# Kernel optimization log

Measured on AMD Instinct MI355X. Metric: run time of the kernel, lower is better.

Reference implementation:

```python
import jax, jax.numpy as jnp
import numpy as np
from jax import lax

K = 9
CENTER = K // 2
EXTEND = 1.0
EPS = 1e-5
GROUPS = 16  # out_ch // 4


def conv2d(x, w, b, stride, padding):
    y = lax.conv_general_dilated(x, w, window_strides=stride, padding=padding,
                                 dimension_numbers=('NCHW', 'OIHW', 'NCHW'))
    return y + b[None, :, None, None]


def setup_inputs() -> dict:
    key = jax.random.key(0)
    ks = jax.random.split(key, 9)
    B, C, Wd, Hd, OUT = 8, 64, 128, 128, 64
    f = jax.random.normal(ks[0], (B, C, Wd, Hd), jnp.float32)
    w_off = jax.random.normal(ks[1], (2 * K, C, 3, 3), jnp.float32) * 0.05
    b_off = jax.random.normal(ks[2], (2 * K,), jnp.float32) * 0.05
    bn_gamma = 1.0 + 0.1 * jax.random.normal(ks[3], (2 * K,), jnp.float32)
    bn_beta = 0.1 * jax.random.normal(ks[4], (2 * K,), jnp.float32)
    w_dsc = jax.random.normal(ks[5], (OUT, C, K, 1), jnp.float32) * 0.05
    b_dsc = jax.random.normal(ks[6], (OUT,), jnp.float32) * 0.05
    gn_gamma = 1.0 + 0.1 * jax.random.normal(ks[7], (OUT,), jnp.float32)
    gn_beta = 0.1 * jax.random.normal(ks[8], (OUT,), jnp.float32)
    return {'f': f, 'w_off': w_off, 'b_off': b_off, 'bn_gamma': bn_gamma,
            'bn_beta': bn_beta, 'w_dsc': w_dsc, 'b_dsc': b_dsc,
            'gn_gamma': gn_gamma, 'gn_beta': gn_beta}


def _forward(f, w_off, b_off, bn_gamma, bn_beta, w_dsc, b_dsc, gn_gamma, gn_beta):
    B, C, Wd, Hd = f.shape  # module names: width=shape[2], height=shape[3]
    dt = f.dtype

    # offset branch: conv3x3 -> BatchNorm (training mode, batch stats) -> tanh
    off = conv2d(f, w_off, b_off, (1, 1), 'SAME')
    mu = off.mean(axis=(0, 2, 3), keepdims=True)
    var = off.var(axis=(0, 2, 3), keepdims=True)
    off = (off - mu) / jnp.sqrt(var + EPS)
    off = off * bn_gamma[None, :, None, None] + bn_beta[None, :, None, None]
    off = jnp.tanh(off)

    y_off = off[:, :K]  # [B,K,Wd,Hd]; x_off (off[:, K:]) unused for morph=0

    # cumulative offset scan from the center point (morph=0).
    # NOTE: endpoints 0 and K-1 keep detached raw offsets (torch detach().clone()).
    raw0 = lax.stop_gradient(y_off)
    offn = [None] * K
    offn[CENTER] = jnp.zeros_like(y_off[:, 0])
    for i in range(1, CENTER):
        offn[CENTER + i] = offn[CENTER + i - 1] + y_off[:, CENTER + i]
        offn[CENTER - i] = offn[CENTER - i + 1] + y_off[:, CENTER - i]
    offn[0] = raw0[:, 0]
    offn[K - 1] = raw0[:, K - 1]
    offn = jnp.stack(offn, axis=1)  # [B,K,Wd,Hd]

    # coordinate grids: y indexes the width axis, x the height axis
    y_new = jnp.arange(Wd, dtype=dt)[None, None, :, None] + offn * EXTEND  # [B,K,Wd,Hd]
    x_new = ((jnp.arange(K, dtype=dt) - CENTER)[None, :, None, None]
             + jnp.arange(Hd, dtype=dt)[None, None, None, :])  # [1,K,1,Hd]
    x_new = jnp.broadcast_to(x_new, (B, K, Wd, Hd))

    # layout [B, K*Wd, Hd] via (B,K,Wd,Hd) -> (B,Wd,K,Hd)
    y_s = jnp.transpose(y_new, (0, 2, 1, 3)).reshape(B, K * Wd * Hd)
    x_s = jnp.transpose(x_new, (0, 2, 1, 3)).reshape(B, K * Wd * Hd)

    # bilinear interpolation (clamped corner indices, unclamped y/x in weights)
    y0 = jnp.floor(y_s).astype(jnp.int32)
    x0 = jnp.floor(x_s).astype(jnp.int32)
    y0c = jnp.clip(y0, 0, Wd - 1)
    y1c = jnp.clip(y0 + 1, 0, Wd - 1)
    x0c = jnp.clip(x0, 0, Hd - 1)
    x1c = jnp.clip(x0 + 1, 0, Hd - 1)

    feat = jnp.transpose(f, (0, 2, 3, 1)).reshape(B, Wd * Hd, C)

    def gather(yi, xi):
        idx = (yi * Hd + xi)[:, :, None]  # [B,N,1]
        return jnp.take_along_axis(feat, idx, axis=1)  # [B,N,C]

    va0 = gather(y0c, x0c)
    vc0 = gather(y0c, x1c)
    va1 = gather(y1c, x0c)
    vc1 = gather(y1c, x1c)

    y0f, y1f = y0c.astype(dt), y1c.astype(dt)
    x0f, x1f = x0c.astype(dt), x1c.astype(dt)
    wa = ((y1f - y_s) * (x1f - x_s))[:, :, None]
    wb = ((y1f - y_s) * (x_s - x0f))[:, :, None]
    wc = ((y_s - y0f) * (x1f - x_s))[:, :, None]
    wd = ((y_s - y0f) * (x_s - x0f))[:, :, None]

    out = va0 * wa + vc0 * wb + va1 * wc + vc1 * wd  # [B,N,C]
    deformed = jnp.transpose(out.reshape(B, K * Wd, Hd, C), (0, 3, 1, 2))  # [B,C,K*Wd,Hd]

    # strided conv over the K snake points -> [B,OUT,Wd,Hd]
    x = conv2d(deformed, w_dsc, b_dsc, (K, 1), 'VALID')

    # GroupNorm + ReLU
    OUT = x.shape[1]
    xg = x.reshape(B, GROUPS, -1)
    gmu = xg.mean(axis=-1, keepdims=True)
    gvar = xg.var(axis=-1, keepdims=True)
    xg = (xg - gmu) / jnp.sqrt(gvar + EPS)
    x = xg.reshape(x.shape) * gn_gamma[None, :, None, None] + gn_beta[None, :, None, None]
    return jax.nn.relu(x)


def reference(f, w_off, b_off, bn_gamma, bn_beta, w_dsc, b_dsc, gn_gamma, gn_beta):
    return _forward(f, w_off, b_off, bn_gamma, bn_beta, w_dsc, b_dsc, gn_gamma, gn_beta)
```

## Files before the change

kernel.cpp:

```cpp
#include <hip/hip_runtime.h>

#define B_   8
#define C_   64
#define W_   128
#define H_   128
#define K_   9
#define OUT_ 64
#define NPIX (B_*W_*H_)
#define EPS_ 1e-5f

typedef __attribute__((ext_vector_type(8))) short bf16x8;
typedef __attribute__((ext_vector_type(4))) float f32x4;

#define FEATBF_OFF  0
#define XPRE_OFF    4194304
#define OFFPRE_OFF  8388608
#define OFFH_OFF    9568256
#define WT_OFF      14286848
#define WP_OFF      14305280
#define BNSTATS_OFF 14310464
#define GSTATS_OFF  14310500
#define STATS_BYTES ((18+18+256+256)*sizeof(float))

__device__ __forceinline__ unsigned pack2bf(float a, float b) {
    union { float f; unsigned u; } ua, ub;
    ua.f = a; ub.f = b;
    unsigned x = ua.u, y = ub.u;
    x += 0x7fffu + ((x >> 16) & 1u);
    y += 0x7fffu + ((y >> 16) & 1u);
    return (x >> 16) | (y & 0xffff0000u);
}
__device__ __forceinline__ float bflo(unsigned u) {
    union { unsigned u; float f; } v; v.u = u << 16; return v.f;
}
__device__ __forceinline__ float bfhi(unsigned u) {
    union { unsigned u; float f; } v; v.u = u & 0xffff0000u; return v.f;
}

__global__ __launch_bounds__(256) void k_nhwc(const float* __restrict__ f,
                                              unsigned short* __restrict__ featbf) {
    __shared__ float tile[64][65];
    int bid = blockIdx.x;
    int ht = bid & 1;
    int w  = (bid >> 1) & 127;
    int b  = bid >> 8;
    int t  = threadIdx.x;
    int lh = t & 63;
    int c0 = (t >> 6) * 16;
    const float* fp = f + (((b*64)*128 + w)*128) + ht*64 + lh;
#pragma unroll
    for (int i = 0; i < 16; i++) {
        int c = c0 + i;
        tile[c][lh] = fp[c*16384];
    }
    __syncthreads();
    int lc = t & 63;
    int h0 = (t >> 6) * 16;
    unsigned short* obf = featbf + ((size_t)((b*128 + w)*128) + ht*64)*64 + lc;
#pragma unroll
    for (int i = 0; i < 16; i++) {
        int hr = h0 + i;
        union { float f; unsigned u; } v; v.f = tile[lc][hr];
        unsigned x = v.u + 0x7fffu + ((v.u >> 16) & 1u);
        obf[(size_t)hr*64] = (unsigned short)(x >> 16);
    }
}

__global__ void k_wprep(const float* __restrict__ w_dsc, unsigned short* __restrict__ wTbf,
                        const float* __restrict__ w_off, float* __restrict__ wP) {
    int bid = blockIdx.x;
    if (bid < 144) {
        int i = bid*256 + threadIdx.x;
        if (i >= 9*64*64) return;
        int c = i & 63;
        int o = (i >> 6) & 63;
        int k = i >> 12;
        union { float f; unsigned u; } v;
        v.f = w_dsc[(o*64 + c)*9 + k];
        unsigned x = v.u + 0x7fffu + ((v.u >> 16) & 1u);
        wTbf[i] = (unsigned short)(x >> 16);
    } else {
        int i = (bid-144)*256 + threadIdx.x;
        if (i >= 64*81) return;
        int c    = i / 81;
        int rem  = i % 81;
        int dw   = rem / 27;
        int rem2 = rem % 27;
        int ck   = rem2 / 3;
        int dh   = rem2 % 3;
        wP[i] = w_off[ck*576 + c*9 + dw*3 + dh];
    }
}

__global__ __launch_bounds__(128) void k_conv_off(const float* __restrict__ f,
                                                  const float* __restrict__ wP,
                                                  float* __restrict__ off_half) {
    int t   = threadIdx.x;
    int bid = blockIdx.x;
    int b   = bid & 7;
    int w   = (bid >> 3) & 127;
    int cq  = bid >> 10;
    int h   = t;

    float em = (h == 0)   ? 0.f : 1.f;
    float ep = (h == 127) ? 0.f : 1.f;

    const float* fb = f + (size_t)b*1048576 + (size_t)(cq*16)*16384 + (size_t)w*128;
    const float* wb = wP + cq*16*81;

    float acc[9];
#pragma unroll
    for (int ck = 0; ck < 9; ck++) acc[ck] = 0.f;

#pragma unroll 4
    for (int c = 0; c < 16; c++) {
        const float* p  = fb + c*16384;
        const float* wc = wb + c*81;
#pragma unroll
        for (int dw = -1; dw <= 1; dw++) {
            int wy = w + dw;
            if ((unsigned)wy < 128u) {
                const float* q = p + dw*128;
                float v1 = q[h];
                float v0 = __shfl_up(v1, 1);
                float v2 = __shfl_down(v1, 1);
                if (t == 64) v0 = q[63];
                if (t == 63) v2 = q[64];
                v0 *= em; v2 *= ep;
                const float* ww = wc + (dw+1)*27;
#pragma unroll
                for (int ck = 0; ck < 9; ck++)
                    acc[ck] += v0*ww[ck*3] + v1*ww[ck*3+1] + v2*ww[ck*3+2];
            }
        }
    }

    float* dst = off_half + (size_t)cq*1179648;
    int pixoff = (w << 7) + h;
#pragma unroll
    for (int ck = 0; ck < 9; ck++)
        dst[((b*9 + ck) << 14) + pixoff] = acc[ck];
}

__global__ __launch_bounds__(256) void k_bn_stats(const float* __restrict__ off_half,
                                                  float* __restrict__ off_pre,
                                                  float* __restrict__ bnstats) {
    __shared__ float wred[4][2];
    int bid = blockIdx.x;
    int b  = bid / 36;
    int rem = bid % 36;
    int ck = rem / 4;
    int wq = rem % 4;
    int t  = threadIdx.x;
    int base4 = (((b*9+ck) << 14) + wq*4096) >> 2;

    const float4* h0 = (const float4*)off_half;
    const float4* h1 = (const float4*)(off_half + 1179648);
    const float4* h2 = (const float4*)(off_half + 2359296);
    const float4* h3 = (const float4*)(off_half + 3538944);
    float4* op = (float4*)off_pre;

    float s = 0.f, q = 0.f;
#pragma unroll
    for (int i = 0; i < 4; i++) {
        int idx = base4 + t + i*256;
        float4 a = h0[idx], bb = h1[idx], cc = h2[idx], dd = h3[idx];
        float4 v;
        v.x = (a.x + bb.x) + (cc.x + dd.x);
        v.y = (a.y + bb.y) + (cc.y + dd.y);
        v.z = (a.z + bb.z) + (cc.z + dd.z);
        v.w = (a.w + bb.w) + (cc.w + dd.w);
        op[idx] = v;
        s += v.x + v.y + v.z + v.w;
        q += v.x*v.x + v.y*v.y + v.z*v.z + v.w*v.w;
    }
    for (int off = 32; off; off >>= 1) {
        s += __shfl_down(s, off);
        q += __shfl_down(q, off);
    }
    if ((t & 63) == 0) { wred[t >> 6][0] = s; wred[t >> 6][1] = q; }
    __syncthreads();
    if (t == 0) atomicAdd(&bnstats[ck*2],   wred[0][0]+wred[1][0]+wred[2][0]+wred[3][0]);
    if (t == 1) atomicAdd(&bnstats[ck*2+1], wred[0][1]+wred[1][1]+wred[2][1]+wred[3][1]);
}

__global__ __launch_bounds__(256) void k_sample_dsc(const unsigned short* __restrict__ featbf,
                                                    const float* __restrict__ off_pre,
                                                    const float* __restrict__ bnstats,
                                                    const float* __restrict__ bn_gamma,
                                                    const float* __restrict__ bn_beta,
                                                    const unsigned short* __restrict__ wTbf,
                                                    const float* __restrict__ b_dsc,
                                                    unsigned short* __restrict__ xprebf,
                                                    float* __restrict__ gstats) {
    __shared__ __align__(16) unsigned char lds_samp[128*128];
    __shared__ __align__(16) unsigned char lds_wk[64*128];
    __shared__ float ynew[9][128];
    __shared__ float red[16][2];
    __shared__ float bnab[18];

    int t = threadIdx.x;
    int b = blockIdx.x & 7, w = blockIdx.x >> 3;

    if (t < 9) {
        float n    = (float)NPIX;
        float mean = bnstats[t*2] / n;
        float var  = bnstats[t*2+1] / n - mean*mean;
        float A    = bn_gamma[t] / sqrtf(var + EPS_);
        bnab[t*2]   = A;
        bnab[t*2+1] = bn_beta[t] - mean * A;
    }
    if (t < 16) { red[t][0] = 0.f; red[t][1] = 0.f; }
    __syncthreads();

    if (t < 128) {
        int h = t;
        float y[9];
#pragma unroll
        for (int ck = 0; ck < 9; ck++) {
            float v = off_pre[((b*9+ck) << 14) + (w << 7) + h];
            y[ck] = tanhf(bnab[ck*2]*v + bnab[ck*2+1]);
        }
        float ofn[9];
        ofn[4] = 0.f;
        ofn[5] = y[5]; ofn[6] = y[5]+y[6]; ofn[7] = y[5]+y[6]+y[7];
        ofn[3] = y[3]; ofn[2] = y[3]+y[2]; ofn[1] = y[3]+y[2]+y[1];
        ofn[0] = y[0]; ofn[8] = y[8];
#pragma unroll
        for (int k = 0; k < 9; k++) ynew[k][h] = (float)w + ofn[k];
    }

    f32x4 acc[2][4];
#pragma unroll
    for (int mi = 0; mi < 2; mi++)
#pragma unroll
        for (int ni = 0; ni < 4; ni++) {
            acc[mi][ni][0] = 0.f; acc[mi][ni][1] = 0.f;
            acc[mi][ni][2] = 0.f; acc[mi][ni][3] = 0.f;
        }

    int lane = t & 63, wv = t >> 6;
    int m0 = wv * 32;
    int lm = lane & 15, lk = lane >> 4;
    int hs = t >> 1;
    int cq = (t & 1) * 4;

    uint4 wv0, wv1;
    {
        const uint4* src = (const uint4*)wTbf;
        wv0 = src[t];
        wv1 = src[t + 256];
    }

    __syncthreads();

    for (int k = 0; k < 9; k++) {
        if (k) __syncthreads();

        {
#pragma unroll
            for (int i = 0; i < 2; i++) {
                int ci = t + i*256;
                uint4 v = (i == 0) ? wv0 : wv1;
                int o  = ci >> 3;
                int cb = (ci & 7) << 4;
                *(uint4*)(lds_wk + o*128 + (cb ^ ((o & 7) << 4))) = v;
            }
        }

        {
            int x0 = k - 4 + hs;
            unsigned char* dst = lds_samp + hs*128;
            int bcol0 = (t & 1) * 64;
            if ((unsigned)x0 < 127u) {
                float ys = ynew[k][hs];
                int y0  = (int)floorf(ys);
                int y0c = min(max(y0, 0), 127), y1c = min(max(y0+1, 0), 127);
                float wa = (float)y1c - ys;
                float wc = ys - (float)y0c;
                const unsigned short* pb = featbf + ((size_t)b << 20);
                const uint4* p0 = (const uint4*)(pb + (y0c*128 + x0)*64) + cq;
                const uint4* p1 = (const uint4*)(pb + (y1c*128 + x0)*64) + cq;
#pragma unroll
                for (int ci = 0; ci < 4; ci++) {
                    uint4 a = p0[ci], c = p1[ci];
                    uint4 u;
                    u.x = pack2bf(bflo(a.x)*wa + bflo(c.x)*wc, bfhi(a.x)*wa + bfhi(c.x)*wc);
                    u.y = pack2bf(bflo(a.y)*wa + bflo(c.y)*wc, bfhi(a.y)*wa + bfhi(c.y)*wc);
                    u.z = pack2bf(bflo(a.z)*wa + bflo(c.z)*wc, bfhi(a.z)*wa + bfhi(c.z)*wc);
                    u.w = pack2bf(bflo(a.w)*wa + bflo(c.w)*wc, bfhi(a.w)*wa + bfhi(c.w)*wc);
                    *(uint4*)(dst + ((bcol0 + ci*16) ^ ((hs & 7) << 4))) = u;
                }
            } else {
                uint4 z = make_uint4(0,0,0,0);
#pragma unroll
                for (int ci = 0; ci < 4; ci++)
                    *(uint4*)(dst + ((bcol0 + ci*16) ^ ((hs & 7) << 4))) = z;
            }
        }

        if (k < 8) {
            const uint4* src = (const uint4*)(wTbf + ((k+1) << 12));
            wv0 = src[t];
            wv1 = src[t + 256];
        }
        __syncthreads();

#pragma unroll
        for (int ks = 0; ks < 2; ks++) {
            bf16x8 af[2], bfr[4];
#pragma unroll
            for (int mi = 0; mi < 2; mi++) {
                int h = m0 + mi*16 + lm;
                af[mi] = *(const bf16x8*)(lds_samp + h*128 + ((ks*64 + lk*16) ^ ((h & 7) << 4)));
            }
#pragma unroll
            for (int ni = 0; ni < 4; ni++) {
                int o = ni*16 + lm;
                bfr[ni] = *(const bf16x8*)(lds_wk + o*128 + ((ks*64 + lk*16) ^ ((o & 7) << 4)));
            }
#pragma unroll
            for (int mi = 0; mi < 2; mi++)
#pragma unroll
                for (int ni = 0; ni < 4; ni++)
                    acc[mi][ni] = __builtin_amdgcn_mfma_f32_16x16x32_bf16(af[mi], bfr[ni], acc[mi][ni], 0, 0, 0);
        }
    }

#pragma unroll
    for (int ni = 0; ni < 4; ni++) {
        int o = ni*16 + lm;
        float bias = b_dsc[o];
        float s1 = 0.f, s2 = 0.f;
#pragma unroll
        for (int mi = 0; mi < 2; mi++) {
            float4 r;
            r.x = acc[mi][ni][0] + bias;
            r.y = acc[mi][ni][1] + bias;
            r.z = acc[mi][ni][2] + bias;
            r.w = acc[mi][ni][3] + bias;
            s1 += r.x + r.y + r.z + r.w;
            s2 += r.x*r.x + r.y*r.y + r.z*r.z + r.w*r.w;
            int h = m0 + mi*16 + lk*4;
            uint2 u2;
            u2.x = pack2bf(r.x, r.y);
            u2.y = pack2bf(r.z, r.w);
            *(uint2*)(xprebf + (((b*64 + o) << 14) + (w << 7) + h)) = u2;
        }
        s1 += __shfl_xor(s1, 1);  s1 += __shfl_xor(s1, 2);
        s1 += __shfl_xor(s1, 16); s1 += __shfl_xor(s1, 32);
        s2 += __shfl_xor(s2, 1);  s2 += __shfl_xor(s2, 2);
        s2 += __shfl_xor(s2, 16); s2 += __shfl_xor(s2, 32);
        if (lk == 0 && (lm & 3) == 0) {
            atomicAdd(&red[ni*4 + (lm >> 2)][0], s1);
            atomicAdd(&red[ni*4 + (lm >> 2)][1], s2);
        }
    }
    __syncthreads();
    if (t < 16) {
        atomicAdd(&gstats[(b*16 + t)*2],   red[t][0]);
        atomicAdd(&gstats[(b*16 + t)*2+1], red[t][1]);
    }
}

__global__ __launch_bounds__(256) void k_gn_apply(const unsigned short* __restrict__ xprebf,
                                                  const float* __restrict__ gstats,
                                                  const float* __restrict__ gn_gamma,
                                                  const float* __restrict__ gn_beta,
                                                  float* __restrict__ out) {
    int i8  = blockIdx.x*256 + threadIdx.x;
    int idx = i8 * 8;
    int o = (idx >> 14) & 63;
    int b = idx >> 20;
    int g = o >> 2;
    float n    = 65536.f;
    float mean = gstats[(b*16+g)*2] / n;
    float var  = gstats[(b*16+g)*2+1] / n - mean*mean;
    float istd = 1.0f / sqrtf(var + EPS_);
    float ga = gn_gamma[o] * istd;
    float be = gn_beta[o] - mean * ga;
    uint4 v = *(const uint4*)(xprebf + idx);
    float4 r0, r1;
    r0.x = fmaxf(bflo(v.x)*ga + be, 0.f);
    r0.y = fmaxf(bfhi(v.x)*ga + be, 0.f);
    r0.z = fmaxf(bflo(v.y)*ga + be, 0.f);
    r0.w = fmaxf(bfhi(v.y)*ga + be, 0.f);
    r1.x = fmaxf(bflo(v.z)*ga + be, 0.f);
    r1.y = fmaxf(bfhi(v.z)*ga + be, 0.f);
    r1.z = fmaxf(bflo(v.w)*ga + be, 0.f);
    r1.w = fmaxf(bfhi(v.w)*ga + be, 0.f);
    *(float4*)(out + idx)     = r0;
    *(float4*)(out + idx + 4) = r1;
}

extern "C" void kernel_launch(void* const* d_in, const int* in_sizes, int n_in,
                              void* d_out, int out_size, void* d_ws, size_t ws_size,
                              hipStream_t stream) {
    const float* f        = (const float*)d_in[0];
    const float* w_off    = (const float*)d_in[1];
    const float* bn_gamma = (const float*)d_in[3];
    const float* bn_beta  = (const float*)d_in[4];
    const float* w_dsc    = (const float*)d_in[5];
    const float* b_dsc    = (const float*)d_in[6];
    const float* gn_gamma = (const float*)d_in[7];
    const float* gn_beta  = (const float*)d_in[8];

    float* ws      = (float*)d_ws;
    unsigned short* featbf = (unsigned short*)(ws + FEATBF_OFF);
    unsigned short* xprebf = (unsigned short*)(ws + XPRE_OFF);
    float* off_pre = ws + OFFPRE_OFF;
    float* off_half= ws + OFFH_OFF;
    unsigned short* wTbf = (unsigned short*)(ws + WT_OFF);
    float* wP      = ws + WP_OFF;
    float* bnstats = ws + BNSTATS_OFF;
    float* gstats  = ws + GSTATS_OFF;

    hipMemsetAsync(bnstats, 0, STATS_BYTES, stream);

    k_nhwc<<<2048, 256, 0, stream>>>(f, featbf);
    k_wprep<<<165, 256, 0, stream>>>(w_dsc, wTbf, w_off, wP);
    k_conv_off<<<4096, 128, 0, stream>>>(f, wP, off_half);
    k_bn_stats<<<288, 256, 0, stream>>>(off_half, off_pre, bnstats);
    k_sample_dsc<<<1024, 256, 0, stream>>>(featbf, off_pre, bnstats, bn_gamma, bn_beta,
                                           wTbf, b_dsc, xprebf, gstats);
    k_gn_apply<<<4096, 256, 0, stream>>>(xprebf, gstats, gn_gamma, gn_beta, (float*)d_out);
}
```

Measured before the change: 126.3 us.

## Fuse NHWC bf16 transpose into offset conv launch and split sample tiles by half-row

The standalone NHWC/bf16 conversion kernel is removed. Its work now runs in 1024 extra blocks of the offset-conv launch, where each thread reads 64 channels with strided loads and writes packed 16-byte bf16 vectors without an LDS transpose. The sampling+MFMA kernel now handles 64 h-positions per block instead of 128, doubling the grid to 2048 blocks and halving LDS and accumulator use. The aim is to save a launch, overlap the transpose with the conv, and raise occupancy, at the cost of uncoalesced strided reads in the transpose path and more redundant per-k weight staging across blocks.

```diff
diff --git a/kernel.cpp b/kernel.cpp
--- a/kernel.cpp
+++ b/kernel.cpp
@@ -35,35 +35,6 @@
 }
 __device__ __forceinline__ float bfhi(unsigned u) {
     union { unsigned u; float f; } v; v.u = u & 0xffff0000u; return v.f;
-}
-
-__global__ __launch_bounds__(256) void k_nhwc(const float* __restrict__ f,
-                                              unsigned short* __restrict__ featbf) {
-    __shared__ float tile[64][65];
-    int bid = blockIdx.x;
-    int ht = bid & 1;
-    int w  = (bid >> 1) & 127;
-    int b  = bid >> 8;
-    int t  = threadIdx.x;
-    int lh = t & 63;
-    int c0 = (t >> 6) * 16;
-    const float* fp = f + (((b*64)*128 + w)*128) + ht*64 + lh;
-#pragma unroll
-    for (int i = 0; i < 16; i++) {
-        int c = c0 + i;
-        tile[c][lh] = fp[c*16384];
-    }
-    __syncthreads();
-    int lc = t & 63;
-    int h0 = (t >> 6) * 16;
-    unsigned short* obf = featbf + ((size_t)((b*128 + w)*128) + ht*64)*64 + lc;
-#pragma unroll
-    for (int i = 0; i < 16; i++) {
-        int hr = h0 + i;
-        union { float f; unsigned u; } v; v.f = tile[lc][hr];
-        unsigned x = v.u + 0x7fffu + ((v.u >> 16) & 1u);
-        obf[(size_t)hr*64] = (unsigned short)(x >> 16);
-    }
 }
 
 __global__ void k_wprep(const float* __restrict__ w_dsc, unsigned short* __restrict__ wTbf,
@@ -92,54 +63,75 @@
     }
 }
 
-__global__ __launch_bounds__(128) void k_conv_off(const float* __restrict__ f,
-                                                  const float* __restrict__ wP,
-                                                  float* __restrict__ off_half) {
+__global__ __launch_bounds__(128) void k_conv_nhwc(const float* __restrict__ f,
+                                                   const float* __restrict__ wP,
+                                                   float* __restrict__ off_half,
+                                                   unsigned short* __restrict__ featbf) {
     int t   = threadIdx.x;
     int bid = blockIdx.x;
-    int b   = bid & 7;
-    int w   = (bid >> 3) & 127;
-    int cq  = bid >> 10;
-    int h   = t;
-
-    float em = (h == 0)   ? 0.f : 1.f;
-    float ep = (h == 127) ? 0.f : 1.f;
-
-    const float* fb = f + (size_t)b*1048576 + (size_t)(cq*16)*16384 + (size_t)w*128;
-    const float* wb = wP + cq*16*81;
-
-    float acc[9];
-#pragma unroll
-    for (int ck = 0; ck < 9; ck++) acc[ck] = 0.f;
+    if (bid < 4096) {
+        int b   = bid & 7;
+        int w   = (bid >> 3) & 127;
+        int cq  = bid >> 10;
+        int h   = t;
+
+        float em = (h == 0)   ? 0.f : 1.f;
+        float ep = (h == 127) ? 0.f : 1.f;
+
+        const float* fb = f + (size_t)b*1048576 + (size_t)(cq*16)*16384 + (size_t)w*128;
+        const float* wb = wP + cq*16*81;
+
+        float acc[9];
+#pragma unroll
+        for (int ck = 0; ck < 9; ck++) acc[ck] = 0.f;
 
 #pragma unroll 4
-    for (int c = 0; c < 16; c++) {
-        const float* p  = fb + c*16384;
-        const float* wc = wb + c*81;
-#pragma unroll
-        for (int dw = -1; dw <= 1; dw++) {
-            int wy = w + dw;
-            if ((unsigned)wy < 128u) {
-                const float* q = p + dw*128;
-                float v1 = q[h];
-                float v0 = __shfl_up(v1, 1);
-                float v2 = __shfl_down(v1, 1);
-                if (t == 64) v0 = q[63];
-                if (t == 63) v2 = q[64];
-                v0 *= em; v2 *= ep;
-                const float* ww = wc + (dw+1)*27;
-#pragma unroll
-                for (int ck = 0; ck < 9; ck++)
-                    acc[ck] += v0*ww[ck*3] + v1*ww[ck*3+1] + v2*ww[ck*3+2];
+        for (int c = 0; c < 16; c++) {
+            const float* p  = fb + c*16384;
+            const float* wc = wb + c*81;
+#pragma unroll
+            for (int dw = -1; dw <= 1; dw++) {
+                int wy = w + dw;
+                if ((unsigned)wy < 128u) {
+                    const float* q = p + dw*128;
+                    float v1 = q[h];
+                    float v0 = __shfl_up(v1, 1);
+                    float v2 = __shfl_down(v1, 1);
+                    if (t == 64) v0 = q[63];
+                    if (t == 63) v2 = q[64];
+                    v0 *= em; v2 *= ep;
+                    const float* ww = wc + (dw+1)*27;
+#pragma unroll
+                    for (int ck = 0; ck < 9; ck++)
+                        acc[ck] += v0*ww[ck*3] + v1*ww[ck*3+1] + v2*ww[ck*3+2];
+                }
             }
         }
-    }
-
-    float* dst = off_half + (size_t)cq*1179648;
-    int pixoff = (w << 7) + h;
-#pragma unroll
-    for (int ck = 0; ck < 9; ck++)
-        dst[((b*9 + ck) << 14) + pixoff] = acc[ck];
+
+        float* dst = off_half + (size_t)cq*1179648;
+        int pixoff = (w << 7) + h;
+#pragma unroll
+        for (int ck = 0; ck < 9; ck++)
+            dst[((b*9 + ck) << 14) + pixoff] = acc[ck];
+    } else {
+        int nb = bid - 4096;
+        int b  = nb & 7;
+        int w  = nb >> 3;
+        int h  = t;
+        const float* fp = f + (size_t)b*1048576 + (size_t)w*128 + h;
+        unsigned short* obf = featbf + ((size_t)((b*128 + w)*128) + h)*64;
+#pragma unroll 2
+        for (int cc = 0; cc < 64; cc += 8) {
+            float v0 = fp[(cc+0)*16384], v1 = fp[(cc+1)*16384];
+            float v2 = fp[(cc+2)*16384], v3 = fp[(cc+3)*16384];
+            float v4 = fp[(cc+4)*16384], v5 = fp[(cc+5)*16384];
+            float v6 = fp[(cc+6)*16384], v7 = fp[(cc+7)*16384];
+            uint4 u;
+            u.x = pack2bf(v0, v1); u.y = pack2bf(v2, v3);
+            u.z = pack2bf(v4, v5); u.w = pack2bf(v6, v7);
+            *(uint4*)(obf + cc) = u;
+        }
+    }
 }
 
 __global__ __launch_bounds__(256) void k_bn_stats(const float* __restrict__ off_half,
@@ -193,14 +185,16 @@
                                                     const float* __restrict__ b_dsc,
                                                     unsigned short* __restrict__ xprebf,
                                                     float* __restrict__ gstats) {
-    __shared__ __align__(16) unsigned char lds_samp[128*128];
+    __shared__ __align__(16) unsigned char lds_samp[64*128];
     __shared__ __align__(16) unsigned char lds_wk[64*128];
-    __shared__ float ynew[9][128];
+    __shared__ float ynew[9][64];
     __shared__ float red[16][2];
     __shared__ float bnab[18];
 
     int t = threadIdx.x;
-    int b = blockIdx.x & 7, w = blockIdx.x >> 3;
+    int bid = blockIdx.x;
+    int b = bid & 7, w = (bid >> 3) & 127, mh = bid >> 10;
+    int hbase = mh * 64;
 
     if (t < 9) {
         float n    = (float)NPIX;
@@ -213,8 +207,8 @@
     if (t < 16) { red[t][0] = 0.f; red[t][1] = 0.f; }
     __syncthreads();
 
-    if (t < 128) {
-        int h = t;
+    if (t < 64) {
+        int h = hbase + t;
         float y[9];
 #pragma unroll
         for (int ck = 0; ck < 9; ck++) {
@@ -227,23 +221,20 @@
         ofn[3] = y[3]; ofn[2] = y[3]+y[2]; ofn[1] = y[3]+y[2]+y[1];
         ofn[0] = y[0]; ofn[8] = y[8];
 #pragma unroll
-        for (int k = 0; k < 9; k++) ynew[k][h] = (float)w + ofn[k];
-    }
-
-    f32x4 acc[2][4];
-#pragma unroll
-    for (int mi = 0; mi < 2; mi++)
-#pragma unroll
-        for (int ni = 0; ni < 4; ni++) {
-            acc[mi][ni][0] = 0.f; acc[mi][ni][1] = 0.f;
-            acc[mi][ni][2] = 0.f; acc[mi][ni][3] = 0.f;
-        }
+        for (int k = 0; k < 9; k++) ynew[k][t] = (float)w + ofn[k];
+    }
+
+    f32x4 acc[4];
+#pragma unroll
+    for (int ni = 0; ni < 4; ni++) {
+        acc[ni][0] = 0.f; acc[ni][1] = 0.f; acc[ni][2] = 0.f; acc[ni][3] = 0.f;
+    }
 
     int lane = t & 63, wv = t >> 6;
-    int m0 = wv * 32;
+    int m0 = wv * 16;
     int lm = lane & 15, lk = lane >> 4;
-    int hs = t >> 1;
-    int cq = (t & 1) * 4;
+    int hsl = t >> 2;
+    int cq  = t & 3;
 
     uint4 wv0, wv1;
     {
@@ -269,33 +260,34 @@
         }
 
         {
-            int x0 = k - 4 + hs;
-            unsigned char* dst = lds_samp + hs*128;
-            int bcol0 = (t & 1) * 64;
+            int hg = hbase + hsl;
+            int x0 = k - 4 + hg;
+            unsigned char* dst = lds_samp + hsl*128;
+            int bcol0 = cq * 32;
             if ((unsigned)x0 < 127u) {
-                float ys = ynew[k][hs];
+                float ys = ynew[k][hsl];
                 int y0  = (int)floorf(ys);
                 int y0c = min(max(y0, 0), 127), y1c = min(max(y0+1, 0), 127);
                 float wa = (float)y1c - ys;
                 float wc = ys - (float)y0c;
                 const unsigned short* pb = featbf + ((size_t)b << 20);
-                const uint4* p0 = (const uint4*)(pb + (y0c*128 + x0)*64) + cq;
-                const uint4* p1 = (const uint4*)(pb + (y1c*128 + x0)*64) + cq;
-#pragma unroll
-                for (int ci = 0; ci < 4; ci++) {
+                const uint4* p0 = (const uint4*)(pb + (y0c*128 + x0)*64) + cq*2;
+                const uint4* p1 = (const uint4*)(pb + (y1c*128 + x0)*64) + cq*2;
+#pragma unroll
+                for (int ci = 0; ci < 2; ci++) {
                     uint4 a = p0[ci], c = p1[ci];
                     uint4 u;
                     u.x = pack2bf(bflo(a.x)*wa + bflo(c.x)*wc, bfhi(a.x)*wa + bfhi(c.x)*wc);
                     u.y = pack2bf(bflo(a.y)*wa + bflo(c.y)*wc, bfhi(a.y)*wa + bfhi(c.y)*wc);
                     u.z = pack2bf(bflo(a.z)*wa + bflo(c.z)*wc, bfhi(a.z)*wa + bfhi(c.z)*wc);
                     u.w = pack2bf(bflo(a.w)*wa + bflo(c.w)*wc, bfhi(a.w)*wa + bfhi(c.w)*wc);
-                    *(uint4*)(dst + ((bcol0 + ci*16) ^ ((hs & 7) << 4))) = u;
+                    *(uint4*)(dst + ((bcol0 + ci*16) ^ ((hsl & 7) << 4))) = u;
                 }
             } else {
                 uint4 z = make_uint4(0,0,0,0);
 #pragma unroll
-                for (int ci = 0; ci < 4; ci++)
-                    *(uint4*)(dst + ((bcol0 + ci*16) ^ ((hs & 7) << 4))) = z;
+                for (int ci = 0; ci < 2; ci++)
+                    *(uint4*)(dst + ((bcol0 + ci*16) ^ ((hsl & 7) << 4))) = z;
             }
         }
 
@@ -308,11 +300,10 @@
 
 #pragma unroll
         for (int ks = 0; ks < 2; ks++) {
-            bf16x8 af[2], bfr[4];
-#pragma unroll
-            for (int mi = 0; mi < 2; mi++) {
-                int h = m0 + mi*16 + lm;
-                af[mi] = *(const bf16x8*)(lds_samp + h*128 + ((ks*64 + lk*16) ^ ((h & 7) << 4)));
+            bf16x8 af, bfr[4];
+            {
+                int hl = m0 + lm;
+                af = *(const bf16x8*)(lds_samp + hl*128 + ((ks*64 + lk*16) ^ ((hl & 7) << 4)));
             }
 #pragma unroll
             for (int ni = 0; ni < 4; ni++) {
@@ -320,10 +311,8 @@
                 bfr[ni] = *(const bf16x8*)(lds_wk + o*128 + ((ks*64 + lk*16) ^ ((o & 7) << 4)));
             }
 #pragma unroll
-            for (int mi = 0; mi < 2; mi++)
-#pragma unroll
-                for (int ni = 0; ni < 4; ni++)
-                    acc[mi][ni] = __builtin_amdgcn_mfma_f32_16x16x32_bf16(af[mi], bfr[ni], acc[mi][ni], 0, 0, 0);
+            for (int ni = 0; ni < 4; ni++)
+                acc[ni] = __builtin_amdgcn_mfma_f32_16x16x32_bf16(af, bfr[ni], acc[ni], 0, 0, 0);
         }
     }
 
@@ -331,22 +320,19 @@
     for (int ni = 0; ni < 4; ni++) {
         int o = ni*16 + lm;
         float bias = b_dsc[o];
-        float s1 = 0.f, s2 = 0.f;
-#pragma unroll
-        for (int mi = 0; mi < 2; mi++) {
-            float4 r;
-            r.x = acc[mi][ni][0] + bias;
-            r.y = acc[mi][ni][1] + bias;
-            r.z = acc[mi][ni][2] + bias;
-            r.w = acc[mi][ni][3] + bias;
-            s1 += r.x + r.y + r.z + r.w;
-            s2 += r.x*r.x + r.y*r.y + r.z*r.z + r.w*r.w;
-            int h = m0 + mi*16 + lk*4;
-            uint2 u2;
-            u2.x = pack2bf(r.x, r.y);
-            u2.y = pack2bf(r.z, r.w);
-            *(uint2*)(xprebf + (((b*64 + o) << 14) + (w << 7) + h)) = u2;
-        }
+        float4 r;
+        r.x = acc[ni][0] + bias;
+        r.y = acc[ni][1] + bias;
+        r.z = acc[ni][2] + bias;
+        r.w = acc[ni][3] + bias;
+        float s1 = r.x + r.y + r.z + r.w;
+        float s2 = r.x*r.x + r.y*r.y + r.z*r.z + r.w*r.w;
+        int hg = hbase + m0 + lk*4;
+        uint2 u2;
+        u2.x = pack2bf(r.x, r.y);
+        u2.y = pack2bf(r.z, r.w);
+        *(uint2*)(xprebf + (((b*64 + o) << 14) + (w << 7) + hg)) = u2;
+
         s1 += __shfl_xor(s1, 1);  s1 += __shfl_xor(s1, 2);
         s1 += __shfl_xor(s1, 16); s1 += __shfl_xor(s1, 32);
         s2 += __shfl_xor(s2, 1);  s2 += __shfl_xor(s2, 2);
@@ -417,11 +403,10 @@
 
     hipMemsetAsync(bnstats, 0, STATS_BYTES, stream);
 
-    k_nhwc<<<2048, 256, 0, stream>>>(f, featbf);
     k_wprep<<<165, 256, 0, stream>>>(w_dsc, wTbf, w_off, wP);
-    k_conv_off<<<4096, 128, 0, stream>>>(f, wP, off_half);
+    k_conv_nhwc<<<5120, 128, 0, stream>>>(f, wP, off_half, featbf);
     k_bn_stats<<<288, 256, 0, stream>>>(off_half, off_pre, bnstats);
-    k_sample_dsc<<<1024, 256, 0, stream>>>(featbf, off_pre, bnstats, bn_gamma, bn_beta,
+    k_sample_dsc<<<2048, 256, 0, stream>>>(featbf, off_pre, bnstats, bn_gamma, bn_beta,
                                            wTbf, b_dsc, xprebf, gstats);
     k_gn_apply<<<4096, 256, 0, stream>>>(xprebf, gstats, gn_gamma, gn_beta, (float*)d_out);
 }
```

Result: slower. 142.0 us (+12.4%).
